# Performance work log

Hardware: AMD Instinct MI355X
Metric: run time of the kernel (lower is better)

Reference implementation:

```python
import jax, jax.numpy as jnp
import numpy as np

IN_F = 128
OUT_F = 64
ALPHA = 0.2  # LeakyReLU negative slope


def setup_inputs() -> dict:
    key = jax.random.key(0)
    k1, k2, k3 = jax.random.split(key, 3)
    B, N = 8, 2048
    inp = jax.random.normal(k1, (B, N, IN_F), dtype=jnp.float32)
    adj = jnp.ones((B, N, N), dtype=jnp.float32)  # unused by the layer (no masking)
    # Parameters (xavier_uniform-style scale)
    w_lim = np.sqrt(6.0 / (IN_F + OUT_F))
    W = jax.random.uniform(k2, (OUT_F, IN_F), minval=-w_lim, maxval=w_lim, dtype=jnp.float32)
    a_lim = np.sqrt(6.0 / (2 * OUT_F + 1))
    a = jax.random.uniform(k3, (1, 2 * OUT_F), minval=-a_lim, maxval=a_lim, dtype=jnp.float32)
    return {"input": inp, "adj": adj, "W": W, "a": a}


def reference(input, adj, W, a):
    # h = W(input): [B, N, OUT_F]
    h = jnp.einsum("bnf,of->bno", input, W)
    # a^T [h_i || h_j] = a1^T h_i + a2^T h_j  (exact decomposition of the concat trick)
    a1 = a[0, :OUT_F]
    a2 = a[0, OUT_F:]
    s1 = jnp.einsum("bno,o->bn", h, a1)  # score contribution from node i
    s2 = jnp.einsum("bno,o->bn", h, a2)  # score contribution from node j
    e = s1[:, :, None] + s2[:, None, :]  # [B, N, N]
    e = jnp.where(e >= 0, e, ALPHA * e)  # LeakyReLU
    attention = jax.nn.softmax(e, axis=2)  # softmax over neighbors j (adj is NOT used)
    h_prime = jnp.einsum("bij,bjo->bio", attention, h)
    # concat=True -> ELU
    return jax.nn.elu(h_prime)
```

## Files before the change

### kernel.cpp

```cpp
#include <hip/hip_runtime.h>
#include <cstdio>

#define ALPHA 0.2f
constexpr int NN = 2048;
constexpr int FI = 128;
constexpr int FO = 64;
constexpr int SEG = 16;
constexpr int NSEG = NN / SEG;

__global__ __launch_bounds__(256) void k_h(const float* __restrict__ inp,
    const float* __restrict__ W, const float* __restrict__ a,
    float* __restrict__ h, float* __restrict__ s1, float* __restrict__ s2)
{
  __shared__ float4 Wq[(FI / 4) * FO];
  const int t = threadIdx.x;
  const float4* Wg = (const float4*)W;
#pragma unroll
  for (int i = 0; i < 8; ++i) {
    int f = t + i * 256;
    int o = f >> 5, cq = f & 31;
    Wq[cq * FO + o] = Wg[f];
  }
  __syncthreads();
  const int lane = t & 63;
  const int wv = t >> 6;
  const size_t rowbase = ((size_t)blockIdx.x * 4 + wv) * 8;
  const float a1v = a[lane], a2v = a[FO + lane];
#pragma unroll
  for (int g = 0; g < 2; ++g) {
    const size_t r0 = rowbase + g * 4;
    const float4* x0 = (const float4*)(inp + r0 * FI);
    const float4* x1 = x0 + (FI / 4);
    const float4* x2 = x0 + 2 * (FI / 4);
    const float4* x3 = x0 + 3 * (FI / 4);
    float acc0 = 0.f, acc1 = 0.f, acc2 = 0.f, acc3 = 0.f;
#pragma unroll
    for (int cq = 0; cq < 32; ++cq) {
      float4 w = Wq[cq * FO + lane];
      float4 xa = x0[cq];
      acc0 = fmaf(xa.x, w.x, fmaf(xa.y, w.y, fmaf(xa.z, w.z, fmaf(xa.w, w.w, acc0))));
      float4 xb = x1[cq];
      acc1 = fmaf(xb.x, w.x, fmaf(xb.y, w.y, fmaf(xb.z, w.z, fmaf(xb.w, w.w, acc1))));
      float4 xc = x2[cq];
      acc2 = fmaf(xc.x, w.x, fmaf(xc.y, w.y, fmaf(xc.z, w.z, fmaf(xc.w, w.w, acc2))));
      float4 xd = x3[cq];
      acc3 = fmaf(xd.x, w.x, fmaf(xd.y, w.y, fmaf(xd.z, w.z, fmaf(xd.w, w.w, acc3))));
    }
    h[(r0 + 0) * FO + lane] = acc0;
    h[(r0 + 1) * FO + lane] = acc1;
    h[(r0 + 2) * FO + lane] = acc2;
    h[(r0 + 3) * FO + lane] = acc3;
    float p0 = acc0 * a1v, q0 = acc0 * a2v;
    float p1 = acc1 * a1v, q1 = acc1 * a2v;
    float p2 = acc2 * a1v, q2 = acc2 * a2v;
    float p3 = acc3 * a1v, q3 = acc3 * a2v;
#pragma unroll
    for (int off = 32; off; off >>= 1) {
      p0 += __shfl_down(p0, off); q0 += __shfl_down(q0, off);
      p1 += __shfl_down(p1, off); q1 += __shfl_down(q1, off);
      p2 += __shfl_down(p2, off); q2 += __shfl_down(q2, off);
      p3 += __shfl_down(p3, off); q3 += __shfl_down(q3, off);
    }
    if (lane == 0) {
      s1[r0 + 0] = p0; s2[r0 + 0] = q0;
      s1[r0 + 1] = p1; s2[r0 + 1] = q1;
      s1[r0 + 2] = p2; s2[r0 + 2] = q2;
      s1[r0 + 3] = p3; s2[r0 + 3] = q3;
    }
  }
}

__global__ __launch_bounds__(256) void k_rankA(const float* __restrict__ s2,
    int* __restrict__ part, float* __restrict__ m2g)
{
  __shared__ float ck[64];
  __shared__ float red[256];
  const int b = blockIdx.x >> 5;
  const int c = blockIdx.x & 31;
  const int t = threadIdx.x;
  if (t < 64) ck[t] = s2[b * NN + c * 64 + t];
  float v[8];
  float mymax = -1e30f;
#pragma unroll
  for (int rr = 0; rr < 8; ++rr) {
    v[rr] = s2[b * NN + rr * 256 + t];
    mymax = fmaxf(mymax, v[rr]);
  }
  red[t] = mymax;
  __syncthreads();
  for (int off = 128; off; off >>= 1) {
    if (t < off) red[t] = fmaxf(red[t], red[t + off]);
    __syncthreads();
  }
  if (c == 0 && t == 0) m2g[b] = red[0];
  int cnt[8] = {0, 0, 0, 0, 0, 0, 0, 0};
  const int j0 = c * 64;
#pragma unroll 4
  for (int jj = 0; jj < 64; ++jj) {
    const float x = ck[jj];
    const int j = j0 + jj;
#pragma unroll
    for (int rr = 0; rr < 8; ++rr) {
      const int i = rr * 256 + t;
      cnt[rr] += (x > v[rr]) || (x == v[rr] && j < i);
    }
  }
  int* pp = part + (size_t)(b * 32 + c) * NN;
#pragma unroll
  for (int rr = 0; rr < 8; ++rr) pp[rr * 256 + t] = cnt[rr];
}

__global__ __launch_bounds__(256) void k_rankB(const float* __restrict__ s2,
    const int* __restrict__ part, const float* __restrict__ m2g,
    float* __restrict__ sortedS2, int* __restrict__ sortedIdx,
    float* __restrict__ ep, float* __restrict__ eq)
{
  const int b = blockIdx.x >> 3;
  const int pr = blockIdx.x & 7;
  const int t = threadIdx.x;
  const int i = pr * 256 + t;
  const int* pp = part + (size_t)b * 32 * NN + i;
  int rank = 0;
#pragma unroll 8
  for (int c = 0; c < 32; ++c) rank += pp[(size_t)c * NN];
  const float v = s2[b * NN + i];
  const float m2 = m2g[b];
  sortedS2[b * NN + rank] = v;
  sortedIdx[b * NN + rank] = i;
  ep[b * NN + rank] = expf(v - m2);
  eq[b * NN + rank] = expf(ALPHA * (v - m2));
}

__global__ __launch_bounds__(256) void k_seg(const float* __restrict__ h,
    const int* __restrict__ sortedIdx, const float* __restrict__ ep,
    const float* __restrict__ eq,
    float* __restrict__ Lp, float* __restrict__ Lq,
    float* __restrict__ segTotP, float* __restrict__ segTotQ)
{
  const int lane = threadIdx.x & 63;
  const int s = blockIdx.x * 4 + (threadIdx.x >> 6);
  const int b = s >> 7;
  const int base = b * NN + (s & (NSEG - 1)) * SEG;
  float hv[SEG], wp[SEG], wq[SEG];
#pragma unroll
  for (int r = 0; r < SEG; ++r) {
    int idx = sortedIdx[base + r];
    hv[r] = h[((size_t)(b * NN + idx)) * FO + lane];
  }
#pragma unroll
  for (int r = 0; r < SEG; ++r) { wp[r] = ep[base + r]; wq[r] = eq[base + r]; }
  float run = 0.f;
#pragma unroll
  for (int r = 0; r < SEG; ++r) {
    run = fmaf(wp[r], hv[r], run);
    Lp[(size_t)(base + r) * FO + lane] = run;
  }
  segTotP[(size_t)s * FO + lane] = run;
  run = 0.f;
#pragma unroll
  for (int r = SEG - 1; r >= 0; --r) {
    run = fmaf(wq[r], hv[r], run);
    Lq[(size_t)(base + r) * FO + lane] = run;
  }
  segTotQ[(size_t)s * FO + lane] = run;
}

__global__ __launch_bounds__(1024) void k_mid(
    const float* __restrict__ ep, const float* __restrict__ eq,
    const float* __restrict__ sortedS2, const float* __restrict__ s1g,
    const float* __restrict__ segTotP, const float* __restrict__ segTotQ,
    float* __restrict__ Zp, float* __restrict__ Zq,
    float* __restrict__ segOffP, float* __restrict__ segOffQ,
    int* __restrict__ kArr)
{
  const int b = blockIdx.x;
  const int t = threadIdx.x;
  const int lane = t & 63;
  const int w = t >> 6;
  __shared__ float ss[NN];
  __shared__ float wt[16], wo[16];
  __shared__ float qs[8][64];

  ss[t] = sortedS2[b * NN + t];
  ss[t + 1024] = sortedS2[b * NN + t + 1024];

  float a0 = ep[b * NN + 2 * t], a1 = ep[b * NN + 2 * t + 1];
  float l = a0 + a1;
  float incl = l;
#pragma unroll
  for (int off = 1; off < 64; off <<= 1) {
    float x = __shfl_up(incl, off);
    if (lane >= off) incl += x;
  }
  if (lane == 63) wt[w] = incl;
  __syncthreads();
  if (t < 16) {
    float v = wt[t];
    float wi = v;
#pragma unroll
    for (int off = 1; off < 16; off <<= 1) {
      float x = __shfl_up(wi, off);
      if (t >= off) wi += x;
    }
    wo[t] = wi - v;
  }
  __syncthreads();
  {
    float excl = wo[w] + (incl - l);
    Zp[b * (NN + 1) + 2 * t] = excl;
    Zp[b * (NN + 1) + 2 * t + 1] = excl + a0;
    if (t == 1023) Zp[b * (NN + 1) + NN] = excl + l;
  }
  __syncthreads();
  float b0 = eq[b * NN + (NN - 1 - 2 * t)], b1 = eq[b * NN + (NN - 2 - 2 * t)];
  float l2 = b0 + b1;
  float incl2 = l2;
#pragma unroll
  for (int off = 1; off < 64; off <<= 1) {
    float x = __shfl_up(incl2, off);
    if (lane >= off) incl2 += x;
  }
  if (lane == 63) wt[w] = incl2;
  __syncthreads();
  if (t < 16) {
    float v = wt[t];
    float wi = v;
#pragma unroll
    for (int off = 1; off < 16; off <<= 1) {
      float x = __shfl_up(wi, off);
      if (t >= off) wi += x;
    }
    wo[t] = wi - v;
  }
  __syncthreads();
  {
    float excl = wo[w] + (incl2 - l2);
    Zq[b * (NN + 1) + NN - 1 - 2 * t] = excl + b0;
    Zq[b * (NN + 1) + NN - 2 - 2 * t] = excl + l2;
    if (t == 0) Zq[b * (NN + 1) + NN] = 0.f;
  }
#pragma unroll
  for (int rr = 0; rr < 2; ++rr) {
    int i = 2 * t + rr;
    float thr = -s1g[b * NN + i];
    int lo = 0, hi = NN;
    while (lo < hi) {
      int mid = (lo + hi) >> 1;
      if (ss[mid] >= thr) lo = mid + 1; else hi = mid;
    }
    kArr[b * NN + i] = lo;
  }
  if (t < 512) {
    const bool isP = t < 256;
    const int o = t & 63;
    const int q = (t >> 6) & 3;
    const float* tot = (isP ? segTotP : segTotQ) + (size_t)b * NSEG * FO + o;
    float ssum = 0.f;
    for (int s = q * 32; s < q * 32 + 32; ++s) ssum += tot[(size_t)s * FO];
    qs[t >> 6][o] = ssum;
  }
  __syncthreads();
  if (t < 512) {
    const bool isP = t < 256;
    const int o = t & 63;
    const int q = (t >> 6) & 3;
    const float* tot = (isP ? segTotP : segTotQ) + (size_t)b * NSEG * FO + o;
    float* off = (isP ? segOffP : segOffQ) + (size_t)b * NSEG * FO + o;
    if (isP) {
      float run = 0.f;
      for (int q2 = 0; q2 < q; ++q2) run += qs[q2][o];
      for (int s = q * 32; s < q * 32 + 32; ++s) {
        off[(size_t)s * FO] = run;
        run += tot[(size_t)s * FO];
      }
    } else {
      float run = 0.f;
      for (int q2 = q + 1; q2 < 4; ++q2) run += qs[4 + q2][o];
      for (int s = q * 32 + 31; s >= q * 32; --s) {
        off[(size_t)s * FO] = run;
        run += tot[(size_t)s * FO];
      }
    }
  }
}

__global__ __launch_bounds__(256) void k_out(const float* __restrict__ s1g,
    const int* __restrict__ kArr,
    const float* __restrict__ Lp, const float* __restrict__ Lq,
    const float* __restrict__ Zp, const float* __restrict__ Zq,
    const float* __restrict__ segOffP, const float* __restrict__ segOffQ,
    const float* __restrict__ m2g, float* __restrict__ out)
{
  const int lane = threadIdx.x & 63;
  const int i = blockIdx.x * 4 + (threadIdx.x >> 6);
  const int b = i >> 11;
  const int k = kArr[i];
  const float s1v = s1g[i];
  const float u = s1v + m2g[b];
  const float c = fmaxf(u, ALPHA * u);
  const float wp = expf(u - c);
  const float wq = expf(ALPHA * u - c);
  const float zp = Zp[b * (NN + 1) + k];
  const float zq = Zq[b * (NN + 1) + k];
  float P = 0.f, Q = 0.f;
  if (k > 0)
    P = segOffP[((size_t)b * NSEG + ((k - 1) >> 4)) * FO + lane] +
        Lp[((size_t)b * NN + (k - 1)) * FO + lane];
  if (k < NN)
    Q = segOffQ[((size_t)b * NSEG + (k >> 4)) * FO + lane] +
        Lq[((size_t)b * NN + k) * FO + lane];
  const float v = (wp * P + wq * Q) / (wp * zp + wq * zq);
  out[(size_t)i * FO + lane] = (v > 0.f) ? v : expm1f(v);
}

extern "C" void kernel_launch(void* const* d_in, const int* in_sizes, int n_in,
                              void* d_out, int out_size, void* d_ws, size_t ws_size,
                              hipStream_t stream) {
  const float* inp = (const float*)d_in[0];
  const float* W = (const float*)d_in[2];
  const float* a = (const float*)d_in[3];
  float* out = (float*)d_out;

  constexpr size_t NH = (size_t)8 * NN * FO;
  constexpr size_t NR = (size_t)8 * NN;
  constexpr size_t NZ = (size_t)8 * (NN + 1);
  constexpr size_t NST = (size_t)8 * NSEG * FO;
  constexpr size_t needFloats = 3 * NH + 7 * NR + 2 * NZ + 4 * NST + 8 + 32 * NR;
  if (ws_size < needFloats * sizeof(float)) {
    fprintf(stderr, "kernel_launch: ws too small (%zu < %zu)\n",
            ws_size, needFloats * sizeof(float));
    return;
  }
  float* ws = (float*)d_ws;
  float* h        = ws;
  float* Lp       = h + NH;
  float* Lq       = Lp + NH;
  float* s1       = Lq + NH;
  float* s2       = s1 + NR;
  float* sortedS2 = s2 + NR;
  int*   sortedIdx= (int*)(sortedS2 + NR);
  float* ep       = (float*)(sortedIdx + NR);
  float* eq       = ep + NR;
  int*   kArr     = (int*)(eq + NR);
  float* Zp       = (float*)(kArr + NR);
  float* Zq       = Zp + NZ;
  float* segTotP  = Zq + NZ;
  float* segTotQ  = segTotP + NST;
  float* segOffP  = segTotQ + NST;
  float* segOffQ  = segOffP + NST;
  float* m2       = segOffQ + NST;
  int*   part     = (int*)(m2 + 8);

  k_h<<<512, 256, 0, stream>>>(inp, W, a, h, s1, s2);
  k_rankA<<<256, 256, 0, stream>>>(s2, part, m2);
  k_rankB<<<64, 256, 0, stream>>>(s2, part, m2, sortedS2, sortedIdx, ep, eq);
  k_seg<<<256, 256, 0, stream>>>(h, sortedIdx, ep, eq, Lp, Lq, segTotP, segTotQ);
  k_mid<<<8, 1024, 0, stream>>>(ep, eq, sortedS2, s1, segTotP, segTotQ,
                                Zp, Zq, segOffP, segOffQ, kArr);
  k_out<<<4096, 256, 0, stream>>>(s1, kArr, Lp, Lq, Zp, Zq,
                                  segOffP, segOffQ, m2, out);
}
```

Baseline: 66.58 us.

## Fuse rank scatter, scans and binary search into one per-batch kernel

Merges k_rankB and k_mid into one per-batch k_batch kernel. It scatters into shared memory, takes the max from sorted position zero instead of a separate reduction, and does the Z scans and binary search from LDS. Segment size grows from 16 to 64. The segment-offset scan moves into k_out, where each block redoes it in shared memory and handles 4 rows per wave. This removes one launch and several global round trips, but k_seg now runs only 64 blocks with a longer serial chain, and k_out repeats the 32-segment scan in every block.

```diff
diff --git a/kernel.cpp b/kernel.cpp
--- a/kernel.cpp
+++ b/kernel.cpp
@@ -5,7 +5,7 @@
 constexpr int NN = 2048;
 constexpr int FI = 128;
 constexpr int FO = 64;
-constexpr int SEG = 16;
+constexpr int SEG = 64;
 constexpr int NSEG = NN / SEG;
 
 __global__ __launch_bounds__(256) void k_h(const float* __restrict__ inp,
@@ -71,28 +71,17 @@
 }
 
 __global__ __launch_bounds__(256) void k_rankA(const float* __restrict__ s2,
-    int* __restrict__ part, float* __restrict__ m2g)
+    int* __restrict__ part)
 {
   __shared__ float ck[64];
-  __shared__ float red[256];
   const int b = blockIdx.x >> 5;
   const int c = blockIdx.x & 31;
   const int t = threadIdx.x;
   if (t < 64) ck[t] = s2[b * NN + c * 64 + t];
   float v[8];
-  float mymax = -1e30f;
-#pragma unroll
-  for (int rr = 0; rr < 8; ++rr) {
-    v[rr] = s2[b * NN + rr * 256 + t];
-    mymax = fmaxf(mymax, v[rr]);
-  }
-  red[t] = mymax;
-  __syncthreads();
-  for (int off = 128; off; off >>= 1) {
-    if (t < off) red[t] = fmaxf(red[t], red[t + off]);
-    __syncthreads();
-  }
-  if (c == 0 && t == 0) m2g[b] = red[0];
+#pragma unroll
+  for (int rr = 0; rr < 8; ++rr) v[rr] = s2[b * NN + rr * 256 + t];
+  __syncthreads();
   int cnt[8] = {0, 0, 0, 0, 0, 0, 0, 0};
   const int j0 = c * 64;
 #pragma unroll 4
@@ -110,25 +99,113 @@
   for (int rr = 0; rr < 8; ++rr) pp[rr * 256 + t] = cnt[rr];
 }
 
-__global__ __launch_bounds__(256) void k_rankB(const float* __restrict__ s2,
-    const int* __restrict__ part, const float* __restrict__ m2g,
+__global__ __launch_bounds__(1024) void k_batch(const float* __restrict__ s2,
+    const int* __restrict__ part, const float* __restrict__ s1g,
     float* __restrict__ sortedS2, int* __restrict__ sortedIdx,
-    float* __restrict__ ep, float* __restrict__ eq)
-{
-  const int b = blockIdx.x >> 3;
-  const int pr = blockIdx.x & 7;
+    float* __restrict__ ep, float* __restrict__ eq,
+    float* __restrict__ Zp, float* __restrict__ Zq,
+    int* __restrict__ kArr, float* __restrict__ m2g)
+{
+  __shared__ float ssv[NN];
+  __shared__ int sid[NN];
+  __shared__ float sep[NN], seq[NN];
+  __shared__ float wt[16], wo[16];
+  const int b = blockIdx.x;
   const int t = threadIdx.x;
-  const int i = pr * 256 + t;
-  const int* pp = part + (size_t)b * 32 * NN + i;
-  int rank = 0;
+  const int lane = t & 63;
+  const int w = t >> 6;
+#pragma unroll
+  for (int rr = 0; rr < 2; ++rr) {
+    const int i = t + rr * 1024;
+    const int* pp = part + (size_t)b * 32 * NN + i;
+    int rank = 0;
 #pragma unroll 8
-  for (int c = 0; c < 32; ++c) rank += pp[(size_t)c * NN];
-  const float v = s2[b * NN + i];
-  const float m2 = m2g[b];
-  sortedS2[b * NN + rank] = v;
-  sortedIdx[b * NN + rank] = i;
-  ep[b * NN + rank] = expf(v - m2);
-  eq[b * NN + rank] = expf(ALPHA * (v - m2));
+    for (int c = 0; c < 32; ++c) rank += pp[(size_t)c * NN];
+    float v = s2[b * NN + i];
+    ssv[rank] = v;
+    sid[rank] = i;
+  }
+  __syncthreads();
+  const float m2 = ssv[0];
+  if (t == 0) m2g[b] = m2;
+#pragma unroll
+  for (int rr = 0; rr < 2; ++rr) {
+    const int r = t + rr * 1024;
+    float v = ssv[r];
+    float e1 = expf(v - m2), e2 = expf(ALPHA * (v - m2));
+    sep[r] = e1; seq[r] = e2;
+    sortedS2[b * NN + r] = v;
+    sortedIdx[b * NN + r] = sid[r];
+    ep[b * NN + r] = e1;
+    eq[b * NN + r] = e2;
+  }
+  __syncthreads();
+  float a0 = sep[2 * t], a1 = sep[2 * t + 1];
+  float l = a0 + a1;
+  float incl = l;
+#pragma unroll
+  for (int off = 1; off < 64; off <<= 1) {
+    float x = __shfl_up(incl, off);
+    if (lane >= off) incl += x;
+  }
+  if (lane == 63) wt[w] = incl;
+  __syncthreads();
+  if (t < 16) {
+    float v = wt[t];
+    float wi = v;
+#pragma unroll
+    for (int off = 1; off < 16; off <<= 1) {
+      float x = __shfl_up(wi, off);
+      if (t >= off) wi += x;
+    }
+    wo[t] = wi - v;
+  }
+  __syncthreads();
+  {
+    float excl = wo[w] + (incl - l);
+    Zp[b * (NN + 1) + 2 * t] = excl;
+    Zp[b * (NN + 1) + 2 * t + 1] = excl + a0;
+    if (t == 1023) Zp[b * (NN + 1) + NN] = excl + l;
+  }
+  __syncthreads();
+  float b0 = seq[NN - 1 - 2 * t], b1 = seq[NN - 2 - 2 * t];
+  float l2 = b0 + b1;
+  float incl2 = l2;
+#pragma unroll
+  for (int off = 1; off < 64; off <<= 1) {
+    float x = __shfl_up(incl2, off);
+    if (lane >= off) incl2 += x;
+  }
+  if (lane == 63) wt[w] = incl2;
+  __syncthreads();
+  if (t < 16) {
+    float v = wt[t];
+    float wi = v;
+#pragma unroll
+    for (int off = 1; off < 16; off <<= 1) {
+      float x = __shfl_up(wi, off);
+      if (t >= off) wi += x;
+    }
+    wo[t] = wi - v;
+  }
+  __syncthreads();
+  {
+    float excl = wo[w] + (incl2 - l2);
+    Zq[b * (NN + 1) + NN - 1 - 2 * t] = excl + b0;
+    Zq[b * (NN + 1) + NN - 2 - 2 * t] = excl + l2;
+    if (t == 0) Zq[b * (NN + 1) + NN] = 0.f;
+  }
+#pragma unroll
+  for (int rr = 0; rr < 2; ++rr) {
+    const int i = 2 * t + rr;
+    const float thr = -s1g[b * NN + i];
+    int lo = 0, hi = NN;
+    while (lo < hi) {
+      int mid = (lo + hi) >> 1;
+      if (ssv[mid] >= thr) lo = mid + 1; else hi = mid;
+    }
+    kArr[b * NN + i] = lo;
+  }
 }
 
 __global__ __launch_bounds__(256) void k_seg(const float* __restrict__ h,
@@ -139,178 +216,85 @@
 {
   const int lane = threadIdx.x & 63;
   const int s = blockIdx.x * 4 + (threadIdx.x >> 6);
-  const int b = s >> 7;
+  const int b = s >> 5;
   const int base = b * NN + (s & (NSEG - 1)) * SEG;
-  float hv[SEG], wp[SEG], wq[SEG];
+  float vq[SEG];
+  float runP = 0.f;
 #pragma unroll
   for (int r = 0; r < SEG; ++r) {
     int idx = sortedIdx[base + r];
-    hv[r] = h[((size_t)(b * NN + idx)) * FO + lane];
-  }
-#pragma unroll
-  for (int r = 0; r < SEG; ++r) { wp[r] = ep[base + r]; wq[r] = eq[base + r]; }
-  float run = 0.f;
-#pragma unroll
-  for (int r = 0; r < SEG; ++r) {
-    run = fmaf(wp[r], hv[r], run);
-    Lp[(size_t)(base + r) * FO + lane] = run;
-  }
-  segTotP[(size_t)s * FO + lane] = run;
-  run = 0.f;
+    float hv = h[((size_t)(b * NN + idx)) * FO + lane];
+    runP = fmaf(ep[base + r], hv, runP);
+    Lp[(size_t)(base + r) * FO + lane] = runP;
+    vq[r] = eq[base + r] * hv;
+  }
+  segTotP[(size_t)s * FO + lane] = runP;
+  float runQ = 0.f;
 #pragma unroll
   for (int r = SEG - 1; r >= 0; --r) {
-    run = fmaf(wq[r], hv[r], run);
-    Lq[(size_t)(base + r) * FO + lane] = run;
-  }
-  segTotQ[(size_t)s * FO + lane] = run;
-}
-
-__global__ __launch_bounds__(1024) void k_mid(
-    const float* __restrict__ ep, const float* __restrict__ eq,
-    const float* __restrict__ sortedS2, const float* __restrict__ s1g,
-    const float* __restrict__ segTotP, const float* __restrict__ segTotQ,
-    float* __restrict__ Zp, float* __restrict__ Zq,
-    float* __restrict__ segOffP, float* __restrict__ segOffQ,
-    int* __restrict__ kArr)
-{
-  const int b = blockIdx.x;
-  const int t = threadIdx.x;
-  const int lane = t & 63;
-  const int w = t >> 6;
-  __shared__ float ss[NN];
-  __shared__ float wt[16], wo[16];
-  __shared__ float qs[8][64];
-
-  ss[t] = sortedS2[b * NN + t];
-  ss[t + 1024] = sortedS2[b * NN + t + 1024];
-
-  float a0 = ep[b * NN + 2 * t], a1 = ep[b * NN + 2 * t + 1];
-  float l = a0 + a1;
-  float incl = l;
-#pragma unroll
-  for (int off = 1; off < 64; off <<= 1) {
-    float x = __shfl_up(incl, off);
-    if (lane >= off) incl += x;
-  }
-  if (lane == 63) wt[w] = incl;
-  __syncthreads();
-  if (t < 16) {
-    float v = wt[t];
-    float wi = v;
-#pragma unroll
-    for (int off = 1; off < 16; off <<= 1) {
-      float x = __shfl_up(wi, off);
-      if (t >= off) wi += x;
-    }
-    wo[t] = wi - v;
-  }
-  __syncthreads();
-  {
-    float excl = wo[w] + (incl - l);
-    Zp[b * (NN + 1) + 2 * t] = excl;
-    Zp[b * (NN + 1) + 2 * t + 1] = excl + a0;
-    if (t == 1023) Zp[b * (NN + 1) + NN] = excl + l;
-  }
-  __syncthreads();
-  float b0 = eq[b * NN + (NN - 1 - 2 * t)], b1 = eq[b * NN + (NN - 2 - 2 * t)];
-  float l2 = b0 + b1;
-  float incl2 = l2;
-#pragma unroll
-  for (int off = 1; off < 64; off <<= 1) {
-    float x = __shfl_up(incl2, off);
-    if (lane >= off) incl2 += x;
-  }
-  if (lane == 63) wt[w] = incl2;
-  __syncthreads();
-  if (t < 16) {
-    float v = wt[t];
-    float wi = v;
-#pragma unroll
-    for (int off = 1; off < 16; off <<= 1) {
-      float x = __shfl_up(wi, off);
-      if (t >= off) wi += x;
-    }
-    wo[t] = wi - v;
-  }
-  __syncthreads();
-  {
-    float excl = wo[w] + (incl2 - l2);
-    Zq[b * (NN + 1) + NN - 1 - 2 * t] = excl + b0;
-    Zq[b * (NN + 1) + NN - 2 - 2 * t] = excl + l2;
-    if (t == 0) Zq[b * (NN + 1) + NN] = 0.f;
-  }
-#pragma unroll
-  for (int rr = 0; rr < 2; ++rr) {
-    int i = 2 * t + rr;
-    float thr = -s1g[b * NN + i];
-    int lo = 0, hi = NN;
-    while (lo < hi) {
-      int mid = (lo + hi) >> 1;
-      if (ss[mid] >= thr) lo = mid + 1; else hi = mid;
-    }
-    kArr[b * NN + i] = lo;
-  }
-  if (t < 512) {
-    const bool isP = t < 256;
-    const int o = t & 63;
-    const int q = (t >> 6) & 3;
-    const float* tot = (isP ? segTotP : segTotQ) + (size_t)b * NSEG * FO + o;
-    float ssum = 0.f;
-    for (int s = q * 32; s < q * 32 + 32; ++s) ssum += tot[(size_t)s * FO];
-    qs[t >> 6][o] = ssum;
-  }
-  __syncthreads();
-  if (t < 512) {
-    const bool isP = t < 256;
-    const int o = t & 63;
-    const int q = (t >> 6) & 3;
-    const float* tot = (isP ? segTotP : segTotQ) + (size_t)b * NSEG * FO + o;
-    float* off = (isP ? segOffP : segOffQ) + (size_t)b * NSEG * FO + o;
-    if (isP) {
-      float run = 0.f;
-      for (int q2 = 0; q2 < q; ++q2) run += qs[q2][o];
-      for (int s = q * 32; s < q * 32 + 32; ++s) {
-        off[(size_t)s * FO] = run;
-        run += tot[(size_t)s * FO];
-      }
-    } else {
-      float run = 0.f;
-      for (int q2 = q + 1; q2 < 4; ++q2) run += qs[4 + q2][o];
-      for (int s = q * 32 + 31; s >= q * 32; --s) {
-        off[(size_t)s * FO] = run;
-        run += tot[(size_t)s * FO];
-      }
-    }
-  }
+    runQ += vq[r];
+    Lq[(size_t)(base + r) * FO + lane] = runQ;
+  }
+  segTotQ[(size_t)s * FO + lane] = runQ;
 }
 
 __global__ __launch_bounds__(256) void k_out(const float* __restrict__ s1g,
     const int* __restrict__ kArr,
     const float* __restrict__ Lp, const float* __restrict__ Lq,
     const float* __restrict__ Zp, const float* __restrict__ Zq,
-    const float* __restrict__ segOffP, const float* __restrict__ segOffQ,
+    const float* __restrict__ segTotP, const float* __restrict__ segTotQ,
     const float* __restrict__ m2g, float* __restrict__ out)
 {
-  const int lane = threadIdx.x & 63;
-  const int i = blockIdx.x * 4 + (threadIdx.x >> 6);
-  const int b = i >> 11;
-  const int k = kArr[i];
-  const float s1v = s1g[i];
-  const float u = s1v + m2g[b];
-  const float c = fmaxf(u, ALPHA * u);
-  const float wp = expf(u - c);
-  const float wq = expf(ALPHA * u - c);
-  const float zp = Zp[b * (NN + 1) + k];
-  const float zq = Zq[b * (NN + 1) + k];
-  float P = 0.f, Q = 0.f;
-  if (k > 0)
-    P = segOffP[((size_t)b * NSEG + ((k - 1) >> 4)) * FO + lane] +
-        Lp[((size_t)b * NN + (k - 1)) * FO + lane];
-  if (k < NN)
-    Q = segOffQ[((size_t)b * NSEG + (k >> 4)) * FO + lane] +
-        Lq[((size_t)b * NN + k) * FO + lane];
-  const float v = (wp * P + wq * Q) / (wp * zp + wq * zq);
-  out[(size_t)i * FO + lane] = (v > 0.f) ? v : expm1f(v);
+  __shared__ float cp[NSEG][FO];
+  __shared__ float cq[NSEG][FO];
+  const int t = threadIdx.x;
+  const int b = blockIdx.x >> 7;
+  const float* stP = segTotP + (size_t)b * NSEG * FO;
+  const float* stQ = segTotQ + (size_t)b * NSEG * FO;
+#pragma unroll
+  for (int i = 0; i < NSEG * FO / 256; ++i) {
+    ((float*)cp)[t + i * 256] = stP[t + i * 256];
+    ((float*)cq)[t + i * 256] = stQ[t + i * 256];
+  }
+  __syncthreads();
+  if (t < 64) {
+    float run = 0.f;
+    for (int ss = 0; ss < NSEG; ++ss) { run += cp[ss][t]; cp[ss][t] = run; }
+  } else if (t < 128) {
+    int o = t - 64;
+    float run = 0.f;
+    for (int ss = NSEG - 1; ss >= 0; --ss) { run += cq[ss][o]; cq[ss][o] = run; }
+  }
+  __syncthreads();
+  const int lane = t & 63;
+  const int wv = t >> 6;
+  const float m2 = m2g[b];
+#pragma unroll
+  for (int rr = 0; rr < 4; ++rr) {
+    const int i = (blockIdx.x & 127) * 16 + wv * 4 + rr;
+    const int gi = b * NN + i;
+    const int k = kArr[gi];
+    const float s1v = s1g[gi];
+    const float u = s1v + m2;
+    const float c = fmaxf(u, ALPHA * u);
+    const float wp = expf(u - c);
+    const float wq = expf(ALPHA * u - c);
+    const float zp = Zp[b * (NN + 1) + k];
+    const float zq = Zq[b * (NN + 1) + k];
+    float P = 0.f, Q = 0.f;
+    if (k > 0) {
+      int sP = (k - 1) >> 6;
+      P = (sP > 0 ? cp[sP - 1][lane] : 0.f) +
+          Lp[((size_t)b * NN + (k - 1)) * FO + lane];
+    }
+    if (k < NN) {
+      int sQ = k >> 6;
+      Q = (sQ < NSEG - 1 ? cq[sQ + 1][lane] : 0.f) +
+          Lq[((size_t)b * NN + k) * FO + lane];
+    }
+    const float v = (wp * P + wq * Q) / (wp * zp + wq * zq);
+    out[(size_t)gi * FO + lane] = (v > 0.f) ? v : expm1f(v);
+  }
 }
 
 extern "C" void kernel_launch(void* const* d_in, const int* in_sizes, int n_in,
@@ -325,7 +309,7 @@
   constexpr size_t NR = (size_t)8 * NN;
   constexpr size_t NZ = (size_t)8 * (NN + 1);
   constexpr size_t NST = (size_t)8 * NSEG * FO;
-  constexpr size_t needFloats = 3 * NH + 7 * NR + 2 * NZ + 4 * NST + 8 + 32 * NR;
+  constexpr size_t needFloats = 3 * NH + 7 * NR + 2 * NZ + 2 * NST + 8 + 32 * NR;
   if (ws_size < needFloats * sizeof(float)) {
     fprintf(stderr, "kernel_launch: ws too small (%zu < %zu)\n",
             ws_size, needFloats * sizeof(float));
@@ -346,17 +330,14 @@
   float* Zq       = Zp + NZ;
   float* segTotP  = Zq + NZ;
   float* segTotQ  = segTotP + NST;
-  float* segOffP  = segTotQ + NST;
-  float* segOffQ  = segOffP + NST;
-  float* m2       = segOffQ + NST;
+  float* m2       = segTotQ + NST;
   int*   part     = (int*)(m2 + 8);
 
   k_h<<<512, 256, 0, stream>>>(inp, W, a, h, s1, s2);
-  k_rankA<<<256, 256, 0, stream>>>(s2, part, m2);
-  k_rankB<<<64, 256, 0, stream>>>(s2, part, m2, sortedS2, sortedIdx, ep, eq);
-  k_seg<<<256, 256, 0, stream>>>(h, sortedIdx, ep, eq, Lp, Lq, segTotP, segTotQ);
-  k_mid<<<8, 1024, 0, stream>>>(ep, eq, sortedS2, s1, segTotP, segTotQ,
-                                Zp, Zq, segOffP, segOffQ, kArr);
-  k_out<<<4096, 256, 0, stream>>>(s1, kArr, Lp, Lq, Zp, Zq,
-                                  segOffP, segOffQ, m2, out);
-}
+  k_rankA<<<256, 256, 0, stream>>>(s2, part);
+  k_batch<<<8, 1024, 0, stream>>>(s2, part, s1, sortedS2, sortedIdx, ep, eq,
+                                  Zp, Zq, kArr, m2);
+  k_seg<<<64, 256, 0, stream>>>(h, sortedIdx, ep, eq, Lp, Lq, segTotP, segTotQ);
+  k_out<<<1024, 256, 0, stream>>>(s1, kArr, Lp, Lq, Zp, Zq,
+                                  segTotP, segTotQ, m2, out);
+}
```

Result: no change. 66.80 us (+0.3%).
